# Kernel optimization log

Hardware: AMD Instinct MI355X
Metric: run time of the kernel (lower is better)

The kernel has to match this reference:

```python
import jax, jax.numpy as jnp
import numpy as np

DIM = 256; SEQ = 2048; WIN = 64; HEADS = 4; RANK = 32; LAYERS = 3; VOCAB = 32000
EPS = 1e-6

def _unit(v):
    # unit_normalize_values: project onto unit sphere along feature dim
    return v / jnp.maximum(jnp.linalg.norm(v, axis=-1, keepdims=True), EPS)

def _signed_softmax(s):
    # signed_softmax_state: sign(s) * softmax(|s|) over nodes
    return jnp.sign(s) * jax.nn.softmax(jnp.abs(s), axis=-1)

def setup_inputs() -> dict:
    key = jax.random.key(0)
    ks = jax.random.split(key, 10)
    d = DIM
    return {
        "input_ids": jax.random.randint(ks[0], (2, SEQ), 0, VOCAB, dtype=jnp.int32),
        "emb": 0.02 * jax.random.normal(ks[1], (VOCAB, d), jnp.float32),
        "pos_emb": 0.02 * jax.random.normal(ks[2], (SEQ, d), jnp.float32),
        "anchor_val": 0.02 * jax.random.normal(ks[3], (d,), jnp.float32),
        "anchor_state": jnp.zeros((), jnp.float32),
        "Ws": 0.02 * jax.random.normal(ks[4], (d,), jnp.float32),
        "bs": jnp.zeros((), jnp.float32),
        "U": 0.02 * jax.random.normal(ks[5], (LAYERS, d, HEADS, RANK), jnp.float32),
        "V": 0.02 * jax.random.normal(ks[6], (LAYERS, d, HEADS, RANK), jnp.float32),
        "W1": 0.02 * jax.random.normal(ks[7], (LAYERS, d, 2 * d), jnp.float32),
        "b1": jnp.zeros((LAYERS, 2 * d), jnp.float32),
        "W2": 0.02 * jax.random.normal(ks[8], (LAYERS, 2 * d, d), jnp.float32),
        "b2": jnp.zeros((LAYERS, d), jnp.float32),
    }

def _forward(emb, pos_emb, anchor_val, anchor_state, Ws, bs, U, V, W1, b1, W2, b2, input_ids):
    B, S = input_ids.shape
    tok = emb[input_ids] + pos_emb[None, :S]          # [B,S,D]
    state_src = tok                                    # state projected from pre-unit-norm values
    tok = _unit(tok)
    tstate = state_src @ Ws + bs                       # [B,S] scalar state per node
    val = jnp.concatenate([jnp.broadcast_to(_unit(anchor_val), (B, 1, DIM)), tok], axis=1)
    state = jnp.concatenate([jnp.broadcast_to(anchor_state, (B, 1)), tstate], axis=1)
    N = S + 1
    offs = jnp.arange(-WIN, WIN + 1)
    idx = jnp.arange(N)[:, None] + offs[None, :]       # [N,K]
    valid = (idx >= 0) & (idx < N)
    idxc = jnp.clip(idx, 0, N - 1)
    inv_sqrt_r = np.float32(1.0 / np.sqrt(RANK))
    for l in range(LAYERS):
        q = jnp.einsum('bnd,dhr->bnhr', val, U[l])
        k = jnp.einsum('bnd,dhr->bnhr', val, V[l])
        knb = k[:, idxc]                               # [B,N,K,H,R] window gather
        s = jnp.einsum('bnhr,bnkhr->bnkh', q, knb) * inv_sqrt_r
        s = s.max(axis=-1)                             # max head-aggregate [B,N,K]
        a = jnp.where(valid, jnp.abs(s), -jnp.inf)
        wgt = jnp.where(valid, jnp.sign(s) * jax.nn.softmax(a, axis=-1), 0.0)  # signed-abs-softmax edges
        dval = jnp.einsum('bnk,bnkd->bnd', wgt, val[:, idxc])
        dstate = jnp.sum(wgt * state[:, idxc], axis=-1)
        # apply_delta: residual + norm(identity) + unit-norm + touched-mask where
        updated = val + dval
        nv = _unit(updated)
        touched = jnp.max(jnp.abs(jax.lax.stop_gradient(dval)), axis=-1, keepdims=True) > 0
        val = jnp.where(touched, nv, updated)
        state = _signed_softmax(state + dstate)
        # residual feed-forward then re-unit-norm
        h = jax.nn.gelu(jnp.einsum('bnd,dh->bnh', val, W1[l]) + b1[l], approximate=False)
        val = _unit(val + jnp.einsum('bnh,hd->bnd', h, W2[l]) + b2[l])
    return state, val

def reference(input_ids, emb, pos_emb, anchor_val, anchor_state, Ws, bs, U, V, W1, b1, W2, b2):
    return _forward(emb, pos_emb, anchor_val, anchor_state, Ws, bs, U, V, W1, b1, W2, b2, input_ids)
```

## Files before the change

### kernel.cpp

```cpp
#include <hip/hip_runtime.h>
#include <hip/hip_bf16.h>
#include <math.h>

#define BB 2
#define SS 2048
#define NN 2049
#define MM (BB*NN)
#define DD 256
#define HR 128
#define NHEAD 4
#define WINW 64
#define DFF 512
#define EPSF 1e-6f
#define TB8 257

typedef __attribute__((ext_vector_type(8))) short bf16x8;
typedef __attribute__((ext_vector_type(4))) float f32x4;

__device__ __forceinline__ float wave_sum(float v) {
    v += __shfl_down(v, 32, 64); v += __shfl_down(v, 16, 64);
    v += __shfl_down(v, 8, 64);  v += __shfl_down(v, 4, 64);
    v += __shfl_down(v, 2, 64);  v += __shfl_down(v, 1, 64);
    return v;
}
__device__ __forceinline__ float wave_max(float v) {
    v = fmaxf(v, __shfl_down(v, 32, 64)); v = fmaxf(v, __shfl_down(v, 16, 64));
    v = fmaxf(v, __shfl_down(v, 8, 64));  v = fmaxf(v, __shfl_down(v, 4, 64));
    v = fmaxf(v, __shfl_down(v, 2, 64));  v = fmaxf(v, __shfl_down(v, 1, 64));
    return v;
}
__device__ __forceinline__ float block_sum(float v, float* red) {
    v = wave_sum(v);
    __syncthreads();
    if ((threadIdx.x & 63) == 0) red[threadIdx.x >> 6] = v;
    __syncthreads();
    return red[0] + red[1] + red[2] + red[3];
}
__device__ __forceinline__ float sgnf(float x) {
    return (x > 0.f) ? 1.f : ((x < 0.f) ? -1.f : 0.f);
}
__device__ __forceinline__ ushort f2b(float x) {
    __hip_bfloat16 h = __float2bfloat16(x);
    return *(ushort*)&h;
}
__device__ __forceinline__ float b2f(ushort u) {
    unsigned int v = ((unsigned int)u) << 16;
    return *(float*)&v;
}
__device__ __forceinline__ void split3(float x, ushort& h, ushort& m, ushort& l) {
    h = f2b(x);
    float r1 = x - b2f(h);
    m = f2b(r1);
    l = f2b(r1 - b2f(m));
}
__device__ __forceinline__ void pack_map(int e, int N, int& k, int& n) {
    int j = e & 7;
    int l = (e >> 3) & 63;
    int c = e >> 9;
    int ntiles = N >> 4;
    int kt = c / ntiles, nt = c - kt * ntiles;
    k = kt * 32 + ((l >> 4) << 3) + j;
    n = nt * 16 + (l & 15);
}
__device__ __forceinline__ void dma16(const ushort* g, ushort* lds) {
    __builtin_amdgcn_global_load_lds(
        (const __attribute__((address_space(1))) unsigned int*)g,
        (__attribute__((address_space(3))) unsigned int*)lds,
        16, 0, 0);
}

__global__ void packall_kernel(const float* __restrict__ W1, const float* __restrict__ W2,
                               const float* __restrict__ U,  const float* __restrict__ V,
                               ushort* __restrict__ W1ph, ushort* __restrict__ W1pl,
                               ushort* __restrict__ W2ph, ushort* __restrict__ W2pl,
                               ushort* __restrict__ U0, ushort* __restrict__ U1,
                               ushort* __restrict__ U2,
                               ushort* __restrict__ V0, ushort* __restrict__ V1,
                               ushort* __restrict__ V2) {
    int idx = blockIdx.x * 256 + threadIdx.x;
    int l = idx / 327680;
    int r = idx - l * 327680;
    if (l >= 3) return;
    int k, n;
    if (r < 131072) {
        int e = r;
        pack_map(e, 512, k, n);
        float s = W1[(size_t)l * 131072 + (size_t)k * 512 + n];
        ushort h = f2b(s);
        W1ph[(size_t)l * 131072 + e] = h;
        W1pl[(size_t)l * 131072 + e] = f2b(s - b2f(h));
    } else if (r < 262144) {
        int e = r - 131072;
        pack_map(e, 256, k, n);
        float s = W2[(size_t)l * 131072 + (size_t)k * 256 + n];
        ushort h = f2b(s);
        W2ph[(size_t)l * 131072 + e] = h;
        W2pl[(size_t)l * 131072 + e] = f2b(s - b2f(h));
    } else if (r < 294912) {
        int e = r - 262144;
        pack_map(e, 128, k, n);
        ushort h, m, lo;
        split3(U[(size_t)l * 32768 + (size_t)k * 128 + n], h, m, lo);
        U0[(size_t)l * 32768 + e] = h;
        U1[(size_t)l * 32768 + e] = m;
        U2[(size_t)l * 32768 + e] = lo;
    } else {
        int e = r - 294912;
        pack_map(e, 128, k, n);
        ushort h, m, lo;
        split3(V[(size_t)l * 32768 + (size_t)k * 128 + n], h, m, lo);
        V0[(size_t)l * 32768 + e] = h;
        V1[(size_t)l * 32768 + e] = m;
        V2[(size_t)l * 32768 + e] = lo;
    }
}

__global__ void embed_kernel(const int* __restrict__ ids,
                             const float* __restrict__ emb,
                             const float* __restrict__ pos,
                             const float* __restrict__ anchor_val,
                             const float* __restrict__ anchor_state,
                             const float* __restrict__ Ws,
                             const float* __restrict__ bs,
                             float* __restrict__ val,
                             ushort* __restrict__ v0, ushort* __restrict__ v1,
                             ushort* __restrict__ v2,
                             float* __restrict__ state) {
    __shared__ float red[4];
    int row = blockIdx.x;
    int t = threadIdx.x;
    int b = row / NN, n = row % NN;
    float e;
    if (n == 0) {
        e = anchor_val[t];
    } else {
        int id = ids[b * SS + (n - 1)];
        e = emb[(size_t)id * DD + t] + pos[(size_t)(n - 1) * DD + t];
    }
    float ss = block_sum(e * e, red);
    float ts = block_sum(e * Ws[t], red);
    float rn = 1.f / fmaxf(sqrtf(ss), EPSF);
    float o = e * rn;
    size_t oi = (size_t)row * DD + t;
    val[oi] = o;
    ushort h, m, lo;
    split3(o, h, m, lo);
    v0[oi] = h; v1[oi] = m; v2[oi] = lo;
    if (t == 0) state[row] = (n == 0) ? anchor_state[0] : (ts + bs[0]);
}

__global__ __launch_bounds__(256, 2)
void proj_kernel(const ushort* __restrict__ X0, const ushort* __restrict__ X1,
                 const ushort* __restrict__ X2,
                 const ushort* __restrict__ U0, const ushort* __restrict__ U1,
                 const ushort* __restrict__ U2,
                 const ushort* __restrict__ V0, const ushort* __restrict__ V1,
                 const ushort* __restrict__ V2,
                 ushort* __restrict__ q0, ushort* __restrict__ q1,
                 ushort* __restrict__ q2,
                 ushort* __restrict__ k0, ushort* __restrict__ k1,
                 ushort* __restrict__ k2) {
    __shared__ __align__(16) ushort stage[2][24 * 512];
    int t = threadIdx.x;
    int w = t >> 6, l = t & 63;
    int lm = l & 15, quad = l >> 4;
    int m0 = blockIdx.x * 16;
    bool isQ = (blockIdx.y == 0);
    const ushort* P0 = isQ ? U0 : V0;
    const ushort* P1 = isQ ? U1 : V1;
    const ushort* P2 = isQ ? U2 : V2;
    const ushort* P[3] = {P0, P1, P2};
    int row0 = m0 + lm; if (row0 > MM - 1) row0 = MM - 1;

    #pragma unroll
    for (int i = 0; i < 6; i++) {
        int c = w * 6 + i;
        int p = c >> 3, ntl = c & 7;
        dma16(P[p] + ((size_t)(0 * 8 + ntl) * 64 + l) * 8,
              &stage[0][c * 512 + l * 8]);
    }
    __syncthreads();

    f32x4 acc[2];
    acc[0] = (f32x4)(0.f); acc[1] = (f32x4)(0.f);
    for (int kt = 0; kt < 8; kt++) {
        int cur = kt & 1;
        if (kt < 7) {
            #pragma unroll
            for (int i = 0; i < 6; i++) {
                int c = w * 6 + i;
                int p = c >> 3, ntl = c & 7;
                dma16(P[p] + ((size_t)((kt + 1) * 8 + ntl) * 64 + l) * 8,
                      &stage[cur ^ 1][c * 512 + l * 8]);
            }
        }
        int ko = kt * 32 + quad * 8;
        bf16x8 a0 = *(const bf16x8*)(X0 + (size_t)row0 * DD + ko);
        bf16x8 a1 = *(const bf16x8*)(X1 + (size_t)row0 * DD + ko);
        bf16x8 a2 = *(const bf16x8*)(X2 + (size_t)row0 * DD + ko);
        #pragma unroll
        for (int jj = 0; jj < 2; jj++) {
            int ntl = w * 2 + jj;
            bf16x8 b0 = *(const bf16x8*)&stage[cur][(0 * 8 + ntl) * 512 + l * 8];
            bf16x8 b1 = *(const bf16x8*)&stage[cur][(1 * 8 + ntl) * 512 + l * 8];
            bf16x8 b2 = *(const bf16x8*)&stage[cur][(2 * 8 + ntl) * 512 + l * 8];
            acc[jj] = __builtin_amdgcn_mfma_f32_16x16x32_bf16(a0, b0, acc[jj], 0, 0, 0);
            acc[jj] = __builtin_amdgcn_mfma_f32_16x16x32_bf16(a0, b1, acc[jj], 0, 0, 0);
            acc[jj] = __builtin_amdgcn_mfma_f32_16x16x32_bf16(a1, b0, acc[jj], 0, 0, 0);
            acc[jj] = __builtin_amdgcn_mfma_f32_16x16x32_bf16(a1, b1, acc[jj], 0, 0, 0);
            acc[jj] = __builtin_amdgcn_mfma_f32_16x16x32_bf16(a0, b2, acc[jj], 0, 0, 0);
            acc[jj] = __builtin_amdgcn_mfma_f32_16x16x32_bf16(a2, b0, acc[jj], 0, 0, 0);
        }
        __syncthreads();
    }
    ushort* o0 = isQ ? q0 : k0;
    ushort* o1 = isQ ? q1 : k1;
    ushort* o2 = isQ ? q2 : k2;
    #pragma unroll
    for (int jj = 0; jj < 2; jj++) {
        int n = (w * 2 + jj) * 16 + lm;
        #pragma unroll
        for (int r = 0; r < 4; r++) {
            int tok = m0 + quad * 4 + r;
            if (tok < MM) {
                ushort h, m, lo;
                split3(acc[jj][r], h, m, lo);
                size_t oi = (size_t)tok * HR + n;
                o0[oi] = h; o1[oi] = m; o2[oi] = lo;
            }
        }
    }
}

__global__ __launch_bounds__(256, 2)
void attn_kernel(const float* __restrict__ val_in,
                 const float* __restrict__ state_in,
                 const ushort* __restrict__ q0, const ushort* __restrict__ q1,
                 const ushort* __restrict__ q2,
                 const ushort* __restrict__ k0, const ushort* __restrict__ k1,
                 const ushort* __restrict__ k2,
                 float* __restrict__ val_out,
                 ushort* __restrict__ vbH, ushort* __restrict__ vbM,
                 float* __restrict__ dstate_out) {
    __shared__ float sc4[NHEAD][8][148];
    __shared__ float wgt2[144][12];
    __shared__ float redS[8][4];
    __shared__ float redM[8][4];

    int b = blockIdx.x / TB8;
    int n0 = (blockIdx.x % TB8) * 8;
    int t = threadIdx.x;
    int w = t >> 6, l = t & 63;
    int lm = l & 15, quad = l >> 4;

    {
        int qrow = n0 + (lm & 7);
        if (qrow > NN - 1) qrow = NN - 1;
        size_t qa = ((size_t)(b * NN + qrow)) * HR + w * 32 + quad * 8;
        bf16x8 a0 = *(const bf16x8*)(q0 + qa);
        bf16x8 a1 = *(const bf16x8*)(q1 + qa);
        bf16x8 a2 = *(const bf16x8*)(q2 + qa);
        bf16x8 kf0[9], kf1[9], kf2[9];
        #pragma unroll
        for (int jt = 0; jt < 9; jt++) {
            int j = n0 - 64 + jt * 16 + lm;
            j = (j < 0) ? 0 : ((j > NN - 1) ? NN - 1 : j);
            size_t ka = ((size_t)(b * NN + j)) * HR + w * 32 + quad * 8;
            kf0[jt] = *(const bf16x8*)(k0 + ka);
            kf1[jt] = *(const bf16x8*)(k1 + ka);
            kf2[jt] = *(const bf16x8*)(k2 + ka);
        }
        #pragma unroll
        for (int jt = 0; jt < 9; jt++) {
            f32x4 acc = (f32x4)(0.f);
            acc = __builtin_amdgcn_mfma_f32_16x16x32_bf16(a0, kf0[jt], acc, 0, 0, 0);
            acc = __builtin_amdgcn_mfma_f32_16x16x32_bf16(a0, kf1[jt], acc, 0, 0, 0);
            acc = __builtin_amdgcn_mfma_f32_16x16x32_bf16(a1, kf0[jt], acc, 0, 0, 0);
            acc = __builtin_amdgcn_mfma_f32_16x16x32_bf16(a1, kf1[jt], acc, 0, 0, 0);
            acc = __builtin_amdgcn_mfma_f32_16x16x32_bf16(a0, kf2[jt], acc, 0, 0, 0);
            acc = __builtin_amdgcn_mfma_f32_16x16x32_bf16(a2, kf0[jt], acc, 0, 0, 0);
            if (quad < 2) {
                #pragma unroll
                for (int r = 0; r < 4; r++)
                    sc4[w][quad * 4 + r][jt * 16 + lm] = acc[r];
            }
        }
    }
    __syncthreads();

    {
        int m = t >> 5, p = t & 31;
        int n = n0 + m;
        bool tokv = (n < NN);
        float sv[5]; bool vv[5];
        float mx = -INFINITY;
        #pragma unroll
        for (int i = 0; i < 5; i++) {
            int tap = p + 32 * i;
            bool inb = (tap < 144);
            int tapc = inb ? tap : 0;
            int j = n0 - 64 + tapc;
            float s0 = sc4[0][m][tapc], s1 = sc4[1][m][tapc];
            float s2 = sc4[2][m][tapc], s3 = sc4[3][m][tapc];
            float s = fmaxf(fmaxf(s0, s1), fmaxf(s2, s3)) * 0.17677669529663687f;
            bool v = inb && tokv && (tap >= m) && (tap <= m + 128) && (j >= 0) && (j < NN);
            sv[i] = s; vv[i] = v;
            if (v) mx = fmaxf(mx, fabsf(s));
        }
        for (int off = 16; off > 0; off >>= 1) mx = fmaxf(mx, __shfl_xor(mx, off, 64));
        float ee[5];
        float sum = 0.f;
        #pragma unroll
        for (int i = 0; i < 5; i++) {
            ee[i] = vv[i] ? expf(fabsf(sv[i]) - mx) : 0.f;
            sum += ee[i];
        }
        for (int off = 16; off > 0; off >>= 1) sum += __shfl_xor(sum, off, 64);
        float inv = (sum > 0.f) ? 1.f / sum : 0.f;
        float ds = 0.f;
        #pragma unroll
        for (int i = 0; i < 5; i++) {
            int tap = p + 32 * i;
            if (tap < 144) {
                float wg = vv[i] ? sgnf(sv[i]) * ee[i] * inv : 0.f;
                wgt2[tap][m] = wg;
                if (vv[i]) ds += wg * state_in[b * NN + (n0 - 64 + tap)];
            }
        }
        for (int off = 16; off > 0; off >>= 1) ds += __shfl_xor(ds, off, 64);
        if (p == 0 && tokv) dstate_out[b * NN + n] = ds;
    }
    __syncthreads();

    {
        int d = (t >> 2) * 4;
        int tg = t & 3;
        int tok0 = tg * 2, tok1 = tg * 2 + 1;
        int jlo = (n0 >= 64) ? 0 : (64 - n0);
        int jhi = NN - 1 - n0 + 64; if (jhi > 135) jhi = 135;
        const float* vbase = val_in + ((size_t)(b * NN + n0 - 64)) * DD + d;
        f32x4 acc0 = (f32x4)(0.f), acc1 = (f32x4)(0.f);
        int jj = jlo;
        for (; jj + 3 <= jhi; jj += 4) {
            f32x4 v0 = *(const f32x4*)(vbase + (size_t)(jj + 0) * DD);
            f32x4 v1 = *(const f32x4*)(vbase + (size_t)(jj + 1) * DD);
            f32x4 v2 = *(const f32x4*)(vbase + (size_t)(jj + 2) * DD);
            f32x4 v3 = *(const f32x4*)(vbase + (size_t)(jj + 3) * DD);
            float wa0 = wgt2[jj + 0][tok0], wa1 = wgt2[jj + 0][tok1];
            float wb0 = wgt2[jj + 1][tok0], wb1 = wgt2[jj + 1][tok1];
            float wc0 = wgt2[jj + 2][tok0], wc1 = wgt2[jj + 2][tok1];
            float wd0 = wgt2[jj + 3][tok0], wd1 = wgt2[jj + 3][tok1];
            #pragma unroll
            for (int c = 0; c < 4; c++) {
                acc0[c] += v0[c] * wa0 + v1[c] * wb0 + v2[c] * wc0 + v3[c] * wd0;
                acc1[c] += v0[c] * wa1 + v1[c] * wb1 + v2[c] * wc1 + v3[c] * wd1;
            }
        }
        for (; jj <= jhi; jj++) {
            f32x4 v = *(const f32x4*)(vbase + (size_t)jj * DD);
            float w0 = wgt2[jj][tok0], w1 = wgt2[jj][tok1];
            #pragma unroll
            for (int c = 0; c < 4; c++) {
                acc0[c] += v[c] * w0;
                acc1[c] += v[c] * w1;
            }
        }
        f32x4 u[2]; f32x4 ac[2]; ac[0] = acc0; ac[1] = acc1;
        #pragma unroll
        for (int ti = 0; ti < 2; ti++) {
            int tok = tg * 2 + ti;
            int n = n0 + tok;
            f32x4 vold = (f32x4)(0.f);
            if (n < NN) vold = *(const f32x4*)(val_in + ((size_t)(b * NN + n)) * DD + d);
            u[ti] = vold + ac[ti];
            float s = u[ti][0]*u[ti][0] + u[ti][1]*u[ti][1] + u[ti][2]*u[ti][2] + u[ti][3]*u[ti][3];
            float mb = fmaxf(fmaxf(fabsf(ac[ti][0]), fabsf(ac[ti][1])),
                             fmaxf(fabsf(ac[ti][2]), fabsf(ac[ti][3])));
            for (int off = 4; off <= 32; off <<= 1) {
                s += __shfl_xor(s, off, 64);
                mb = fmaxf(mb, __shfl_xor(mb, off, 64));
            }
            if ((l >> 2) == 0) { redS[tok][w] = s; redM[tok][w] = mb; }
        }
        __syncthreads();
        #pragma unroll
        for (int ti = 0; ti < 2; ti++) {
            int tok = tg * 2 + ti;
            int n = n0 + tok;
            if (n < NN) {
                float ss = redS[tok][0] + redS[tok][1] + redS[tok][2] + redS[tok][3];
                float mab = fmaxf(fmaxf(redM[tok][0], redM[tok][1]),
                                  fmaxf(redM[tok][2], redM[tok][3]));
                float rn = 1.f / fmaxf(sqrtf(ss), EPSF);
                f32x4 o = u[ti];
                if (mab > 0.f) { o[0] *= rn; o[1] *= rn; o[2] *= rn; o[3] *= rn; }
                size_t oi = ((size_t)(b * NN + n)) * DD + d;
                *(f32x4*)(val_out + oi) = o;
                ushort4 hv, mv;
                {
                    ushort h0 = f2b(o[0]); hv.x = h0; mv.x = f2b(o[0] - b2f(h0));
                    ushort h1 = f2b(o[1]); hv.y = h1; mv.y = f2b(o[1] - b2f(h1));
                    ushort h2 = f2b(o[2]); hv.z = h2; mv.z = f2b(o[2] - b2f(h2));
                    ushort h3 = f2b(o[3]); hv.w = h3; mv.w = f2b(o[3] - b2f(h3));
                }
                *(ushort4*)(vbH + oi) = hv;
                *(ushort4*)(vbM + oi) = mv;
            }
        }
    }
}

__global__ __launch_bounds__(256, 2)
void ffn1_kernel(const ushort* __restrict__ XbH, const ushort* __restrict__ XbM,
                 const ushort* __restrict__ W1h, const ushort* __restrict__ W1l,
                 const float*  __restrict__ b1,
                 ushort* __restrict__ Hh, ushort* __restrict__ Hl,
                 const float* __restrict__ state_in, const float* __restrict__ dstate,
                 float* __restrict__ state_out) {
    __shared__ __align__(16) ushort stage[2][32 * 512];
    int t = threadIdx.x;

    if (blockIdx.x == 257) {
        float* red = (float*)&stage[0][0];
        int b = blockIdx.y;
        float lmax = -INFINITY;
        for (int n = t; n < NN; n += 256) {
            float x = state_in[b * NN + n] + dstate[b * NN + n];
            lmax = fmaxf(lmax, fabsf(x));
        }
        lmax = wave_max(lmax);
        if ((t & 63) == 0) red[t >> 6] = lmax;
        __syncthreads();
        float m = fmaxf(fmaxf(red[0], red[1]), fmaxf(red[2], red[3]));
        float lsum = 0.f;
        for (int n = t; n < NN; n += 256)
            lsum += expf(fabsf(state_in[b * NN + n] + dstate[b * NN + n]) - m);
        lsum = wave_sum(lsum);
        __syncthreads();
        if ((t & 63) == 0) red[4 + (t >> 6)] = lsum;
        __syncthreads();
        float inv = 1.f / (red[4] + red[5] + red[6] + red[7]);
        for (int n = t; n < NN; n += 256) {
            float x = state_in[b * NN + n] + dstate[b * NN + n];
            state_out[b * NN + n] = sgnf(x) * expf(fabsf(x) - m) * inv;
        }
        return;
    }

    int w = t >> 6, l = t & 63;
    int lm = l & 15, quad = l >> 4;
    int m0 = blockIdx.x * 16;
    int nh = blockIdx.y;
    int row0 = m0 + lm; if (row0 > MM - 1) row0 = MM - 1;

    #pragma unroll
    for (int i = 0; i < 8; i++) {
        int c = w * 8 + i;
        int p = c >> 4, ntl = c & 15;
        const ushort* src = (p ? W1l : W1h) + ((size_t)(0 * 32 + nh * 16 + ntl) * 64 + l) * 8;
        dma16(src, &stage[0][c * 512 + l * 8]);
    }
    __syncthreads();

    f32x4 acc[4];
    #pragma unroll
    for (int jj = 0; jj < 4; jj++) acc[jj] = (f32x4)(0.f);

    for (int kt = 0; kt < 8; kt++) {
        int cur = kt & 1;
        if (kt < 7) {
            #pragma unroll
            for (int i = 0; i < 8; i++) {
                int c = w * 8 + i;
                int p = c >> 4, ntl = c & 15;
                const ushort* src = (p ? W1l : W1h) +
                    ((size_t)((kt + 1) * 32 + nh * 16 + ntl) * 64 + l) * 8;
                dma16(src, &stage[cur ^ 1][c * 512 + l * 8]);
            }
        }
        int ko = kt * 32 + quad * 8;
        bf16x8 ah = *(const bf16x8*)(XbH + (size_t)row0 * DD + ko);
        bf16x8 am = *(const bf16x8*)(XbM + (size_t)row0 * DD + ko);
        #pragma unroll
        for (int jj = 0; jj < 4; jj++) {
            int ntl = w * 4 + jj;
            bf16x8 bh = *(const bf16x8*)&stage[cur][ntl * 512 + l * 8];
            bf16x8 bl = *(const bf16x8*)&stage[cur][(16 + ntl) * 512 + l * 8];
            acc[jj] = __builtin_amdgcn_mfma_f32_16x16x32_bf16(ah, bh, acc[jj], 0, 0, 0);
            acc[jj] = __builtin_amdgcn_mfma_f32_16x16x32_bf16(am, bh, acc[jj], 0, 0, 0);
            acc[jj] = __builtin_amdgcn_mfma_f32_16x16x32_bf16(ah, bl, acc[jj], 0, 0, 0);
        }
        __syncthreads();
    }
    #pragma unroll
    for (int jj = 0; jj < 4; jj++) {
        int gn = nh * 256 + (w * 4 + jj) * 16 + lm;
        float bb = b1[gn];
        #pragma unroll
        for (int r = 0; r < 4; r++) {
            int tok = m0 + quad * 4 + r;
            if (tok < MM) {
                float x = acc[jj][r] + bb;
                float g = 0.5f * x * (1.f + erff(x * 0.70710678118654752f));
                ushort gh = f2b(g);
                size_t oi = (size_t)tok * DFF + gn;
                Hh[oi] = gh;
                Hl[oi] = f2b(g - b2f(gh));
            }
        }
    }
}

__global__ __launch_bounds__(256, 2)
void ffn2_kernel(const ushort* __restrict__ Hh, const ushort* __restrict__ Hl,
                 const float*  __restrict__ Xf,
                 const ushort* __restrict__ W2h, const ushort* __restrict__ W2l,
                 const float*  __restrict__ b2,
                 float* __restrict__ Yb) {
    __shared__ __align__(16) ushort stage[2][16 * 512];
    int t = threadIdx.x;
    int w = t >> 6, l = t & 63;
    int lm = l & 15, quad = l >> 4;
    int m0 = blockIdx.x * 16;
    int nh = blockIdx.y;
    int row0 = m0 + lm; if (row0 > MM - 1) row0 = MM - 1;

    #pragma unroll
    for (int i = 0; i < 4; i++) {
        int c = w * 4 + i;
        int p = c >> 3, ntl = c & 7;
        const ushort* src = (p ? W2l : W2h) + ((size_t)(0 * 16 + nh * 8 + ntl) * 64 + l) * 8;
        dma16(src, &stage[0][c * 512 + l * 8]);
    }
    __syncthreads();

    f32x4 acc[2];
    acc[0] = (f32x4)(0.f); acc[1] = (f32x4)(0.f);

    for (int kt = 0; kt < 16; kt++) {
        int cur = kt & 1;
        if (kt < 15) {
            #pragma unroll
            for (int i = 0; i < 4; i++) {
                int c = w * 4 + i;
                int p = c >> 3, ntl = c & 7;
                const ushort* src = (p ? W2l : W2h) +
                    ((size_t)((kt + 1) * 16 + nh * 8 + ntl) * 64 + l) * 8;
                dma16(src, &stage[cur ^ 1][c * 512 + l * 8]);
            }
        }
        int ko = kt * 32 + quad * 8;
        bf16x8 ah = *(const bf16x8*)(Hh + (size_t)row0 * DFF + ko);
        bf16x8 al = *(const bf16x8*)(Hl + (size_t)row0 * DFF + ko);
        #pragma unroll
        for (int jj = 0; jj < 2; jj++) {
            int ntl = w * 2 + jj;
            bf16x8 bh = *(const bf16x8*)&stage[cur][ntl * 512 + l * 8];
            bf16x8 bl = *(const bf16x8*)&stage[cur][(8 + ntl) * 512 + l * 8];
            acc[jj] = __builtin_amdgcn_mfma_f32_16x16x32_bf16(ah, bh, acc[jj], 0, 0, 0);
            acc[jj] = __builtin_amdgcn_mfma_f32_16x16x32_bf16(al, bh, acc[jj], 0, 0, 0);
            acc[jj] = __builtin_amdgcn_mfma_f32_16x16x32_bf16(ah, bl, acc[jj], 0, 0, 0);
        }
        __syncthreads();
    }
    #pragma unroll
    for (int jj = 0; jj < 2; jj++) {
        int gn = nh * 128 + (w * 2 + jj) * 16 + lm;
        float bb = b2[gn];
        #pragma unroll
        for (int r = 0; r < 4; r++) {
            int tok = m0 + quad * 4 + r;
            if (tok < MM) {
                size_t oi = (size_t)tok * DD + gn;
                Yb[oi] = Xf[oi] + acc[jj][r] + bb;
            }
        }
    }
}

__global__ void ffn3_kernel(const float* __restrict__ Yb,
                            float* __restrict__ val_out,
                            ushort* __restrict__ o0, ushort* __restrict__ o1,
                            ushort* __restrict__ o2) {
    int t = threadIdx.x;
    int w = t >> 6, l = t & 63;
    int row = blockIdx.x * 4 + w;
    if (row >= MM) return;
    f32x4 y = *(const f32x4*)(Yb + (size_t)row * DD + l * 4);
    float s = y[0]*y[0] + y[1]*y[1] + y[2]*y[2] + y[3]*y[3];
    #pragma unroll
    for (int off = 1; off < 64; off <<= 1) s += __shfl_xor(s, off, 64);
    float rn = 1.f / fmaxf(sqrtf(s), EPSF);
    f32x4 o;
    o[0] = y[0] * rn; o[1] = y[1] * rn; o[2] = y[2] * rn; o[3] = y[3] * rn;
    size_t oi = (size_t)row * DD + l * 4;
    *(f32x4*)(val_out + oi) = o;
    ushort4 h4, m4, l4;
    ushort hh, mm, ll;
    split3(o[0], hh, mm, ll); h4.x = hh; m4.x = mm; l4.x = ll;
    split3(o[1], hh, mm, ll); h4.y = hh; m4.y = mm; l4.y = ll;
    split3(o[2], hh, mm, ll); h4.z = hh; m4.z = mm; l4.z = ll;
    split3(o[3], hh, mm, ll); h4.w = hh; m4.w = mm; l4.w = ll;
    *(ushort4*)(o0 + oi) = h4;
    *(ushort4*)(o1 + oi) = m4;
    *(ushort4*)(o2 + oi) = l4;
}

extern "C" void kernel_launch(void* const* d_in, const int* in_sizes, int n_in,
                              void* d_out, int out_size, void* d_ws, size_t ws_size,
                              hipStream_t stream) {
    const int*   ids          = (const int*)d_in[0];
    const float* emb          = (const float*)d_in[1];
    const float* pos          = (const float*)d_in[2];
    const float* anchor_val   = (const float*)d_in[3];
    const float* anchor_state = (const float*)d_in[4];
    const float* Ws           = (const float*)d_in[5];
    const float* bs           = (const float*)d_in[6];
    const float* U            = (const float*)d_in[7];
    const float* V            = (const float*)d_in[8];
    const float* W1           = (const float*)d_in[9];
    const float* b1           = (const float*)d_in[10];
    const float* W2           = (const float*)d_in[11];
    const float* b2           = (const float*)d_in[12];
    float* out = (float*)d_out;

    ushort* p = (ushort*)d_ws;
    ushort* vA0 = p; p += (size_t)MM * DD;
    ushort* vA1 = p; p += (size_t)MM * DD;
    ushort* vA2 = p; p += (size_t)MM * DD;
    ushort* vB0 = p; p += (size_t)MM * DD;
    ushort* vB1 = p; p += (size_t)MM * DD;
    ushort* q0b = p; p += (size_t)MM * HR;
    ushort* q1b = p; p += (size_t)MM * HR;
    ushort* q2b = p; p += (size_t)MM * HR;
    ushort* k0b = p; p += (size_t)MM * HR;
    ushort* k1b = p; p += (size_t)MM * HR;
    ushort* k2b = p; p += (size_t)MM * HR;
    ushort* Hh  = p; p += (size_t)MM * DFF;
    ushort* Hl  = p; p += (size_t)MM * DFF;
    ushort* W1ph = p; p += 3 * 131072;
    ushort* W1pl = p; p += 3 * 131072;
    ushort* W2ph = p; p += 3 * 131072;
    ushort* W2pl = p; p += 3 * 131072;
    ushort* U0p = p; p += 3 * 32768;
    ushort* U1p = p; p += 3 * 32768;
    ushort* U2p = p; p += 3 * 32768;
    ushort* V0p = p; p += 3 * 32768;
    ushort* V1p = p; p += 3 * 32768;
    ushort* V2p = p; p += 3 * 32768;
    float* f = (float*)p;
    float* valA = f; f += (size_t)MM * DD;
    float* valB = f; f += (size_t)MM * DD;
    float* st0  = f; f += MM;
    float* st1  = f; f += MM;
    float* dst  = f; f += MM;
    float* Yb   = valA;

    packall_kernel<<<3840, 256, 0, stream>>>(W1, W2, U, V,
                                             W1ph, W1pl, W2ph, W2pl,
                                             U0p, U1p, U2p, V0p, V1p, V2p);

    embed_kernel<<<MM, 256, 0, stream>>>(ids, emb, pos, anchor_val, anchor_state,
                                         Ws, bs, valA, vA0, vA1, vA2, st0);
    float* s_in = st0;
    float* s_out = st1;
    for (int l = 0; l < 3; l++) {
        proj_kernel<<<dim3(257, 2), 256, 0, stream>>>(
            vA0, vA1, vA2,
            U0p + (size_t)l * 32768, U1p + (size_t)l * 32768, U2p + (size_t)l * 32768,
            V0p + (size_t)l * 32768, V1p + (size_t)l * 32768, V2p + (size_t)l * 32768,
            q0b, q1b, q2b, k0b, k1b, k2b);
        attn_kernel<<<BB * TB8, 256, 0, stream>>>(valA, s_in,
                                                  q0b, q1b, q2b, k0b, k1b, k2b,
                                                  valB, vB0, vB1, dst);
        ffn1_kernel<<<dim3(258, 2), 256, 0, stream>>>(
            vB0, vB1,
            W1ph + (size_t)l * 131072, W1pl + (size_t)l * 131072, b1 + (size_t)l * DFF,
            Hh, Hl,
            s_in, dst, (l == 2) ? out : s_out);
        ffn2_kernel<<<dim3(257, 2), 256, 0, stream>>>(
            Hh, Hl, valB,
            W2ph + (size_t)l * 131072, W2pl + (size_t)l * 131072, b2 + (size_t)l * DD,
            Yb);
        ffn3_kernel<<<(MM + 3) / 4, 256, 0, stream>>>(
            Yb, (l == 2) ? (out + MM) : valA, vA0, vA1, vA2);
        float* tmp = s_in; s_in = s_out; s_out = tmp;
    }
}
```

Before: 359.5 us.

## Merge weight packing with embedding and software-pipeline GEMM A-operand loads

Fuses the weight-packing and embedding kernels into one launch, so the two independent prologue jobs run concurrently and one launch is saved. In the proj, ffn1 and ffn2 GEMM kernels, the activation (A) fragment loads are double-buffered into registers one k-step ahead. The __syncthreads calls are replaced by explicit s_waitcnt vmcnt counts plus raw s_barrier, so loads for the next stage stay in flight while the current stage computes. The hand-counted vmcnt values must exactly match the number of outstanding loads; any miscount is a race that can corrupt results. Full unrolling also raises register pressure.

```diff
diff --git a/kernel.cpp b/kernel.cpp
--- a/kernel.cpp
+++ b/kernel.cpp
@@ -69,15 +69,50 @@
         16, 0, 0);
 }
 
-__global__ void packall_kernel(const float* __restrict__ W1, const float* __restrict__ W2,
-                               const float* __restrict__ U,  const float* __restrict__ V,
-                               ushort* __restrict__ W1ph, ushort* __restrict__ W1pl,
-                               ushort* __restrict__ W2ph, ushort* __restrict__ W2pl,
-                               ushort* __restrict__ U0, ushort* __restrict__ U1,
-                               ushort* __restrict__ U2,
-                               ushort* __restrict__ V0, ushort* __restrict__ V1,
-                               ushort* __restrict__ V2) {
-    int idx = blockIdx.x * 256 + threadIdx.x;
+__global__ void pre_kernel(const int* __restrict__ ids,
+                           const float* __restrict__ emb,
+                           const float* __restrict__ pos,
+                           const float* __restrict__ anchor_val,
+                           const float* __restrict__ anchor_state,
+                           const float* __restrict__ Ws,
+                           const float* __restrict__ bs,
+                           float* __restrict__ val,
+                           ushort* __restrict__ v0, ushort* __restrict__ v1,
+                           ushort* __restrict__ v2,
+                           float* __restrict__ state,
+                           const float* __restrict__ W1, const float* __restrict__ W2,
+                           const float* __restrict__ U,  const float* __restrict__ V,
+                           ushort* __restrict__ W1ph, ushort* __restrict__ W1pl,
+                           ushort* __restrict__ W2ph, ushort* __restrict__ W2pl,
+                           ushort* __restrict__ U0, ushort* __restrict__ U1,
+                           ushort* __restrict__ U2,
+                           ushort* __restrict__ V0, ushort* __restrict__ V1,
+                           ushort* __restrict__ V2) {
+    __shared__ float red[4];
+    int bid = blockIdx.x;
+    int t = threadIdx.x;
+    if (bid < MM) {
+        int b = bid / NN, n = bid % NN;
+        float e;
+        if (n == 0) {
+            e = anchor_val[t];
+        } else {
+            int id = ids[b * SS + (n - 1)];
+            e = emb[(size_t)id * DD + t] + pos[(size_t)(n - 1) * DD + t];
+        }
+        float ss = block_sum(e * e, red);
+        float ts = block_sum(e * Ws[t], red);
+        float rn = 1.f / fmaxf(sqrtf(ss), EPSF);
+        float o = e * rn;
+        size_t oi = (size_t)bid * DD + t;
+        val[oi] = o;
+        ushort h, m, lo;
+        split3(o, h, m, lo);
+        v0[oi] = h; v1[oi] = m; v2[oi] = lo;
+        if (t == 0) state[bid] = (n == 0) ? anchor_state[0] : (ts + bs[0]);
+        return;
+    }
+    int idx = (bid - MM) * 256 + t;
     int l = idx / 327680;
     int r = idx - l * 327680;
     if (l >= 3) return;
@@ -115,40 +150,6 @@
     }
 }
 
-__global__ void embed_kernel(const int* __restrict__ ids,
-                             const float* __restrict__ emb,
-                             const float* __restrict__ pos,
-                             const float* __restrict__ anchor_val,
-                             const float* __restrict__ anchor_state,
-                             const float* __restrict__ Ws,
-                             const float* __restrict__ bs,
-                             float* __restrict__ val,
-                             ushort* __restrict__ v0, ushort* __restrict__ v1,
-                             ushort* __restrict__ v2,
-                             float* __restrict__ state) {
-    __shared__ float red[4];
-    int row = blockIdx.x;
-    int t = threadIdx.x;
-    int b = row / NN, n = row % NN;
-    float e;
-    if (n == 0) {
-        e = anchor_val[t];
-    } else {
-        int id = ids[b * SS + (n - 1)];
-        e = emb[(size_t)id * DD + t] + pos[(size_t)(n - 1) * DD + t];
-    }
-    float ss = block_sum(e * e, red);
-    float ts = block_sum(e * Ws[t], red);
-    float rn = 1.f / fmaxf(sqrtf(ss), EPSF);
-    float o = e * rn;
-    size_t oi = (size_t)row * DD + t;
-    val[oi] = o;
-    ushort h, m, lo;
-    split3(o, h, m, lo);
-    v0[oi] = h; v1[oi] = m; v2[oi] = lo;
-    if (t == 0) state[row] = (n == 0) ? anchor_state[0] : (ts + bs[0]);
-}
-
 __global__ __launch_bounds__(256, 2)
 void proj_kernel(const ushort* __restrict__ X0, const ushort* __restrict__ X1,
                  const ushort* __restrict__ X2,
@@ -166,26 +167,37 @@
     int lm = l & 15, quad = l >> 4;
     int m0 = blockIdx.x * 16;
     bool isQ = (blockIdx.y == 0);
-    const ushort* P0 = isQ ? U0 : V0;
-    const ushort* P1 = isQ ? U1 : V1;
-    const ushort* P2 = isQ ? U2 : V2;
-    const ushort* P[3] = {P0, P1, P2};
+    const ushort* P[3];
+    P[0] = isQ ? U0 : V0;
+    P[1] = isQ ? U1 : V1;
+    P[2] = isQ ? U2 : V2;
     int row0 = m0 + lm; if (row0 > MM - 1) row0 = MM - 1;
-
+    const ushort* xb0 = X0 + (size_t)row0 * DD + quad * 8;
+    const ushort* xb1 = X1 + (size_t)row0 * DD + quad * 8;
+    const ushort* xb2 = X2 + (size_t)row0 * DD + quad * 8;
+
+    bf16x8 a0[2], a1[2], a2[2];
+    a0[0] = *(const bf16x8*)(xb0);
+    a1[0] = *(const bf16x8*)(xb1);
+    a2[0] = *(const bf16x8*)(xb2);
     #pragma unroll
     for (int i = 0; i < 6; i++) {
         int c = w * 6 + i;
         int p = c >> 3, ntl = c & 7;
-        dma16(P[p] + ((size_t)(0 * 8 + ntl) * 64 + l) * 8,
+        dma16(P[p] + ((size_t)ntl * 64 + l) * 8,
               &stage[0][c * 512 + l * 8]);
     }
-    __syncthreads();
+    asm volatile("" ::: "memory");
 
     f32x4 acc[2];
     acc[0] = (f32x4)(0.f); acc[1] = (f32x4)(0.f);
+    #pragma unroll
     for (int kt = 0; kt < 8; kt++) {
         int cur = kt & 1;
         if (kt < 7) {
+            a0[cur ^ 1] = *(const bf16x8*)(xb0 + (kt + 1) * 32);
+            a1[cur ^ 1] = *(const bf16x8*)(xb1 + (kt + 1) * 32);
+            a2[cur ^ 1] = *(const bf16x8*)(xb2 + (kt + 1) * 32);
             #pragma unroll
             for (int i = 0; i < 6; i++) {
                 int c = w * 6 + i;
@@ -193,25 +205,25 @@
                 dma16(P[p] + ((size_t)((kt + 1) * 8 + ntl) * 64 + l) * 8,
                       &stage[cur ^ 1][c * 512 + l * 8]);
             }
-        }
-        int ko = kt * 32 + quad * 8;
-        bf16x8 a0 = *(const bf16x8*)(X0 + (size_t)row0 * DD + ko);
-        bf16x8 a1 = *(const bf16x8*)(X1 + (size_t)row0 * DD + ko);
-        bf16x8 a2 = *(const bf16x8*)(X2 + (size_t)row0 * DD + ko);
+            asm volatile("s_waitcnt vmcnt(9)" ::: "memory");
+        } else {
+            asm volatile("s_waitcnt vmcnt(0)" ::: "memory");
+        }
+        __builtin_amdgcn_s_barrier();
         #pragma unroll
         for (int jj = 0; jj < 2; jj++) {
             int ntl = w * 2 + jj;
             bf16x8 b0 = *(const bf16x8*)&stage[cur][(0 * 8 + ntl) * 512 + l * 8];
             bf16x8 b1 = *(const bf16x8*)&stage[cur][(1 * 8 + ntl) * 512 + l * 8];
             bf16x8 b2 = *(const bf16x8*)&stage[cur][(2 * 8 + ntl) * 512 + l * 8];
-            acc[jj] = __builtin_amdgcn_mfma_f32_16x16x32_bf16(a0, b0, acc[jj], 0, 0, 0);
-            acc[jj] = __builtin_amdgcn_mfma_f32_16x16x32_bf16(a0, b1, acc[jj], 0, 0, 0);
-            acc[jj] = __builtin_amdgcn_mfma_f32_16x16x32_bf16(a1, b0, acc[jj], 0, 0, 0);
-            acc[jj] = __builtin_amdgcn_mfma_f32_16x16x32_bf16(a1, b1, acc[jj], 0, 0, 0);
-            acc[jj] = __builtin_amdgcn_mfma_f32_16x16x32_bf16(a0, b2, acc[jj], 0, 0, 0);
-            acc[jj] = __builtin_amdgcn_mfma_f32_16x16x32_bf16(a2, b0, acc[jj], 0, 0, 0);
-        }
-        __syncthreads();
+            acc[jj] = __builtin_amdgcn_mfma_f32_16x16x32_bf16(a0[cur], b0, acc[jj], 0, 0, 0);
+            acc[jj] = __builtin_amdgcn_mfma_f32_16x16x32_bf16(a0[cur], b1, acc[jj], 0, 0, 0);
+            acc[jj] = __builtin_amdgcn_mfma_f32_16x16x32_bf16(a1[cur], b0, acc[jj], 0, 0, 0);
+            acc[jj] = __builtin_amdgcn_mfma_f32_16x16x32_bf16(a1[cur], b1, acc[jj], 0, 0, 0);
+            acc[jj] = __builtin_amdgcn_mfma_f32_16x16x32_bf16(a0[cur], b2, acc[jj], 0, 0, 0);
+            acc[jj] = __builtin_amdgcn_mfma_f32_16x16x32_bf16(a2[cur], b0, acc[jj], 0, 0, 0);
+        }
+        __builtin_amdgcn_s_barrier();
     }
     ushort* o0 = isQ ? q0 : k0;
     ushort* o1 = isQ ? q1 : k1;
@@ -452,23 +464,31 @@
     int m0 = blockIdx.x * 16;
     int nh = blockIdx.y;
     int row0 = m0 + lm; if (row0 > MM - 1) row0 = MM - 1;
-
+    const ushort* xh = XbH + (size_t)row0 * DD + quad * 8;
+    const ushort* xm = XbM + (size_t)row0 * DD + quad * 8;
+
+    bf16x8 ah[2], am[2];
+    ah[0] = *(const bf16x8*)(xh);
+    am[0] = *(const bf16x8*)(xm);
     #pragma unroll
     for (int i = 0; i < 8; i++) {
         int c = w * 8 + i;
         int p = c >> 4, ntl = c & 15;
-        const ushort* src = (p ? W1l : W1h) + ((size_t)(0 * 32 + nh * 16 + ntl) * 64 + l) * 8;
+        const ushort* src = (p ? W1l : W1h) + ((size_t)(nh * 16 + ntl) * 64 + l) * 8;
         dma16(src, &stage[0][c * 512 + l * 8]);
     }
-    __syncthreads();
+    asm volatile("" ::: "memory");
 
     f32x4 acc[4];
     #pragma unroll
     for (int jj = 0; jj < 4; jj++) acc[jj] = (f32x4)(0.f);
 
+    #pragma unroll
     for (int kt = 0; kt < 8; kt++) {
         int cur = kt & 1;
         if (kt < 7) {
+            ah[cur ^ 1] = *(const bf16x8*)(xh + (kt + 1) * 32);
+            am[cur ^ 1] = *(const bf16x8*)(xm + (kt + 1) * 32);
             #pragma unroll
             for (int i = 0; i < 8; i++) {
                 int c = w * 8 + i;
@@ -477,20 +497,21 @@
                     ((size_t)((kt + 1) * 32 + nh * 16 + ntl) * 64 + l) * 8;
                 dma16(src, &stage[cur ^ 1][c * 512 + l * 8]);
             }
-        }
-        int ko = kt * 32 + quad * 8;
-        bf16x8 ah = *(const bf16x8*)(XbH + (size_t)row0 * DD + ko);
-        bf16x8 am = *(const bf16x8*)(XbM + (size_t)row0 * DD + ko);
+            asm volatile("s_waitcnt vmcnt(10)" ::: "memory");
+        } else {
+            asm volatile("s_waitcnt vmcnt(0)" ::: "memory");
+        }
+        __builtin_amdgcn_s_barrier();
         #pragma unroll
         for (int jj = 0; jj < 4; jj++) {
             int ntl = w * 4 + jj;
             bf16x8 bh = *(const bf16x8*)&stage[cur][ntl * 512 + l * 8];
             bf16x8 bl = *(const bf16x8*)&stage[cur][(16 + ntl) * 512 + l * 8];
-            acc[jj] = __builtin_amdgcn_mfma_f32_16x16x32_bf16(ah, bh, acc[jj], 0, 0, 0);
-            acc[jj] = __builtin_amdgcn_mfma_f32_16x16x32_bf16(am, bh, acc[jj], 0, 0, 0);
-            acc[jj] = __builtin_amdgcn_mfma_f32_16x16x32_bf16(ah, bl, acc[jj], 0, 0, 0);
-        }
-        __syncthreads();
+            acc[jj] = __builtin_amdgcn_mfma_f32_16x16x32_bf16(ah[cur], bh, acc[jj], 0, 0, 0);
+            acc[jj] = __builtin_amdgcn_mfma_f32_16x16x32_bf16(am[cur], bh, acc[jj], 0, 0, 0);
+            acc[jj] = __builtin_amdgcn_mfma_f32_16x16x32_bf16(ah[cur], bl, acc[jj], 0, 0, 0);
+        }
+        __builtin_amdgcn_s_barrier();
     }
     #pragma unroll
     for (int jj = 0; jj < 4; jj++) {
@@ -524,22 +545,30 @@
     int m0 = blockIdx.x * 16;
     int nh = blockIdx.y;
     int row0 = m0 + lm; if (row0 > MM - 1) row0 = MM - 1;
-
+    const ushort* xh = Hh + (size_t)row0 * DFF + quad * 8;
+    const ushort* xl = Hl + (size_t)row0 * DFF + quad * 8;
+
+    bf16x8 ah[2], al[2];
+    ah[0] = *(const bf16x8*)(xh);
+    al[0] = *(const bf16x8*)(xl);
     #pragma unroll
     for (int i = 0; i < 4; i++) {
         int c = w * 4 + i;
         int p = c >> 3, ntl = c & 7;
-        const ushort* src = (p ? W2l : W2h) + ((size_t)(0 * 16 + nh * 8 + ntl) * 64 + l) * 8;
+        const ushort* src = (p ? W2l : W2h) + ((size_t)(nh * 8 + ntl) * 64 + l) * 8;
         dma16(src, &stage[0][c * 512 + l * 8]);
     }
-    __syncthreads();
+    asm volatile("" ::: "memory");
 
     f32x4 acc[2];
     acc[0] = (f32x4)(0.f); acc[1] = (f32x4)(0.f);
 
+    #pragma unroll
     for (int kt = 0; kt < 16; kt++) {
         int cur = kt & 1;
         if (kt < 15) {
+            ah[cur ^ 1] = *(const bf16x8*)(xh + (kt + 1) * 32);
+            al[cur ^ 1] = *(const bf16x8*)(xl + (kt + 1) * 32);
             #pragma unroll
             for (int i = 0; i < 4; i++) {
                 int c = w * 4 + i;
@@ -548,20 +577,21 @@
                     ((size_t)((kt + 1) * 16 + nh * 8 + ntl) * 64 + l) * 8;
                 dma16(src, &stage[cur ^ 1][c * 512 + l * 8]);
             }
-        }
-        int ko = kt * 32 + quad * 8;
-        bf16x8 ah = *(const bf16x8*)(Hh + (size_t)row0 * DFF + ko);
-        bf16x8 al = *(const bf16x8*)(Hl + (size_t)row0 * DFF + ko);
+            asm volatile("s_waitcnt vmcnt(6)" ::: "memory");
+        } else {
+            asm volatile("s_waitcnt vmcnt(0)" ::: "memory");
+        }
+        __builtin_amdgcn_s_barrier();
         #pragma unroll
         for (int jj = 0; jj < 2; jj++) {
             int ntl = w * 2 + jj;
             bf16x8 bh = *(const bf16x8*)&stage[cur][ntl * 512 + l * 8];
             bf16x8 bl = *(const bf16x8*)&stage[cur][(8 + ntl) * 512 + l * 8];
-            acc[jj] = __builtin_amdgcn_mfma_f32_16x16x32_bf16(ah, bh, acc[jj], 0, 0, 0);
-            acc[jj] = __builtin_amdgcn_mfma_f32_16x16x32_bf16(al, bh, acc[jj], 0, 0, 0);
-            acc[jj] = __builtin_amdgcn_mfma_f32_16x16x32_bf16(ah, bl, acc[jj], 0, 0, 0);
-        }
-        __syncthreads();
+            acc[jj] = __builtin_amdgcn_mfma_f32_16x16x32_bf16(ah[cur], bh, acc[jj], 0, 0, 0);
+            acc[jj] = __builtin_amdgcn_mfma_f32_16x16x32_bf16(al[cur], bh, acc[jj], 0, 0, 0);
+            acc[jj] = __builtin_amdgcn_mfma_f32_16x16x32_bf16(ah[cur], bl, acc[jj], 0, 0, 0);
+        }
+        __builtin_amdgcn_s_barrier();
     }
     #pragma unroll
     for (int jj = 0; jj < 2; jj++) {
@@ -656,12 +686,11 @@
     float* dst  = f; f += MM;
     float* Yb   = valA;
 
-    packall_kernel<<<3840, 256, 0, stream>>>(W1, W2, U, V,
-                                             W1ph, W1pl, W2ph, W2pl,
-                                             U0p, U1p, U2p, V0p, V1p, V2p);
-
-    embed_kernel<<<MM, 256, 0, stream>>>(ids, emb, pos, anchor_val, anchor_state,
-                                         Ws, bs, valA, vA0, vA1, vA2, st0);
+    pre_kernel<<<MM + 3840, 256, 0, stream>>>(ids, emb, pos, anchor_val, anchor_state,
+                                              Ws, bs, valA, vA0, vA1, vA2, st0,
+                                              W1, W2, U, V,
+                                              W1ph, W1pl, W2ph, W2pl,
+                                              U0p, U1p, U2p, V0p, V1p, V2p);
     float* s_in = st0;
     float* s_out = st1;
     for (int l = 0; l < 3; l++) {
```

Measured after the change: 357.8 us. Within noise of the previous version (-0.5%).
